# Kernel tuning notes

Measured on AMD Instinct MI355X. Metric: run time of the kernel, lower is better.

Reference implementation:

```python
import jax, jax.numpy as jnp
import numpy as np

B, T, K, H = 2, 4096, 512, 8


def setup_inputs() -> dict:
    key = jax.random.key(0)
    ks = jax.random.split(key, 6)
    scale = 1.0 / np.sqrt(K)
    return {
        "x": jax.random.normal(ks[0], (B, T, K), dtype=jnp.float32),
        "padding_mask": jnp.ones((B, T), dtype=jnp.int32),
        "Wq": jax.random.normal(ks[1], (K, K), dtype=jnp.float32) * scale,
        "Wk": jax.random.normal(ks[2], (K, K), dtype=jnp.float32) * scale,
        "Wv": jax.random.normal(ks[3], (K, K), dtype=jnp.float32) * scale,
        "Wu": jax.random.normal(ks[4], (K, K), dtype=jnp.float32) * scale,
        "bu": jnp.zeros((K,), dtype=jnp.float32),
    }


def reference(x, padding_mask, Wq, Wk, Wv, Wu, bu):
    b, t, e = x.shape
    h = H
    s = e // h
    # torch Linear: y = x @ W.T
    q = (x @ Wq.T).reshape(b, t, h, s).transpose(0, 2, 1, 3)  # (b,h,t,s)
    k = (x @ Wk.T).reshape(b, t, h, s).transpose(0, 2, 1, 3)
    v = (x @ Wv.T).reshape(b, t, h, s).transpose(0, 2, 1, 3)
    inv4 = e ** (-0.25)
    q = q * inv4
    k = k * inv4
    dot = jnp.einsum("bhqs,bhks->bhqk", q, k)  # (b,h,t,t)
    neg_inf = jnp.float32(-jnp.inf)
    # causal mask (self.mask == True)
    causal = jnp.triu(jnp.ones((t, t), dtype=bool), k=1)
    dot = jnp.where(causal[None, None], neg_inf, dot)
    # padding mask applied along the QUERY dimension, as in the original
    dot = jnp.where(padding_mask[:, None, :, None] == 0, neg_inf, dot)
    attn = jax.nn.softmax(dot, axis=-1)
    out = jnp.einsum("bhqk,bhks->bhqs", attn, v)  # (b,h,t,s)
    out = out.transpose(0, 2, 1, 3).reshape(b, t, e)
    return out @ Wu.T + bu
```

## Files before the change

### kernel.cpp

```cpp
#include <hip/hip_runtime.h>
#include <hip/hip_bf16.h>

#define BB 2
#define TT 4096
#define KK 512
#define HH 8
#define SS 64
#define MM 8192

typedef __attribute__((ext_vector_type(8))) short bf16x8;
typedef __attribute__((ext_vector_type(4))) float f32x4;
typedef unsigned int u32;
typedef __attribute__((ext_vector_type(2))) u32 u32x2;
typedef __attribute__((ext_vector_type(4))) u32 u32x4;

#define SCL_QK 0.25250488f

static __device__ __forceinline__ u32 cvt2(float lo, float hi) {
    u32 r;
    asm("v_cvt_pk_bf16_f32 %0, %1, %2" : "=v"(r) : "v"(lo), "v"(hi));
    return r;
}

#define GLOAD16(g, l) __builtin_amdgcn_global_load_lds( \
    (const __attribute__((address_space(1))) void*)(g), \
    (__attribute__((address_space(3))) void*)(l), 16, 0, 0)

static __device__ __forceinline__ int rho(int v) {
    return (v & 0x23) | ((v & 0x04) << 2) | ((v & 0x18) >> 1);
}

__global__ __launch_bounds__(256) void cvt_bf16(
    const float* __restrict__ x,
    const float* __restrict__ Wq, const float* __restrict__ Wk,
    const float* __restrict__ Wv, const float* __restrict__ Wu,
    short* __restrict__ xb, short* __restrict__ wb)
{
    const int NX = MM * KK;
    const int NW = KK * KK;
    int idx = blockIdx.x * blockDim.x + threadIdx.x;
    int total = (NX + 4 * NW) >> 3;
    for (int g = idx; g < total; g += gridDim.x * blockDim.x) {
        int e = g << 3;
        const float* src; short* dst; float scl = 1.0f;
        if (e < NX) { src = x + e; dst = xb + e; }
        else {
            int gg = e - NX;
            int wsel = gg >> 18;
            int off = gg & (NW - 1);
            src = (wsel == 0 ? Wq : wsel == 1 ? Wk : wsel == 2 ? Wv : Wu) + off;
            dst = wb + gg;
            if (wsel <= 1) scl = SCL_QK;
        }
        float4 a = *(const float4*)src;
        float4 b = *(const float4*)(src + 4);
        a.x *= scl; a.y *= scl; a.z *= scl; a.w *= scl;
        b.x *= scl; b.y *= scl; b.z *= scl; b.w *= scl;
        u32x4 wv = { cvt2(a.x, a.y), cvt2(a.z, a.w), cvt2(b.x, b.y), cvt2(b.z, b.w) };
        *(u32x4*)dst = wv;
    }
}

__global__ __launch_bounds__(256) void proj_qkv(
    const short* __restrict__ xb, const short* __restrict__ wb,
    short* __restrict__ q, short* __restrict__ k, short* __restrict__ v)
{
    __shared__ short aS[128 * 64];
    __shared__ short bS[128 * 64];
    int nt = blockIdx.x, mt = blockIdx.y, z = blockIdx.z;
    const short* W = wb + (size_t)z * KK * KK;
    short* dst = (z == 0) ? q : ((z == 1) ? k : v);
    bool tr = (z != 2);
    int tid = threadIdx.x, wave = tid >> 6, lane = tid & 63;
    int lr = lane & 15, lg = lane >> 4;
    int wr = wave >> 1, wc = wave & 1;
    int l8 = lane >> 3, c8 = lane & 7;

    const short* Ag = xb + (size_t)(mt * 128) * KK;
    const short* Bg = W + (size_t)(nt * 128) * KK;

    f32x4 acc[4][4];
#pragma unroll
    for (int m = 0; m < 4; ++m)
#pragma unroll
        for (int n = 0; n < 4; ++n) acc[m][n] = (f32x4){0.f, 0.f, 0.f, 0.f};

    for (int k0 = 0; k0 < KK; k0 += 64) {
        __syncthreads();
#pragma unroll
        for (int i = 0; i < 4; ++i) {
            int row = wave * 32 + i * 8 + l8;
            GLOAD16(Ag + (size_t)row * KK + k0 + c8 * 8, &aS[(wave * 32 + i * 8) * 64]);
            GLOAD16(Bg + (size_t)row * KK + k0 + c8 * 8, &bS[(wave * 32 + i * 8) * 64]);
        }
        __syncthreads();
#pragma unroll
        for (int kc = 0; kc < 2; ++kc) {
            bf16x8 af[4], bw[4];
#pragma unroll
            for (int m = 0; m < 4; ++m)
                af[m] = *(const bf16x8*)&aS[(wr * 64 + m * 16 + lr) * 64 + kc * 32 + lg * 8];
#pragma unroll
            for (int n = 0; n < 4; ++n)
                bw[n] = *(const bf16x8*)&bS[(wc * 64 + n * 16 + lr) * 64 + kc * 32 + lg * 8];
            if (tr) {
#pragma unroll
                for (int m = 0; m < 4; ++m)
#pragma unroll
                    for (int n = 0; n < 4; ++n)
                        acc[m][n] = __builtin_amdgcn_mfma_f32_16x16x32_bf16(bw[n], af[m], acc[m][n], 0, 0, 0);
            } else {
#pragma unroll
                for (int m = 0; m < 4; ++m)
#pragma unroll
                    for (int n = 0; n < 4; ++n)
                        acc[m][n] = __builtin_amdgcn_mfma_f32_16x16x32_bf16(af[m], bw[n], acc[m][n], 0, 0, 0);
            }
        }
    }

    if (tr) {
        int h = nt * 2 + wc;
#pragma unroll
        for (int n = 0; n < 4; ++n) {
            int s0 = n * 16 + lg * 4;
#pragma unroll
            for (int m = 0; m < 4; ++m) {
                int tg = mt * 128 + wr * 64 + m * 16 + lr;
                int b = tg >> 12, t = tg & (TT - 1);
                u32x2 pk = { cvt2(acc[m][n][0], acc[m][n][1]), cvt2(acc[m][n][2], acc[m][n][3]) };
                *(u32x2*)&dst[((size_t)(b * HH + h) * TT + t) * SS + s0] = pk;
            }
        }
    } else {
#pragma unroll
        for (int n = 0; n < 4; ++n) {
            int nn = nt * 128 + wc * 64 + n * 16 + lr;
            int h = nn >> 6, s = nn & 63;
#pragma unroll
            for (int m = 0; m < 4; ++m) {
                int m0 = mt * 128 + wr * 64 + m * 16 + lg * 4;
                int b = m0 >> 12, t0 = m0 & (TT - 1);
                u32x2 pk = { cvt2(acc[m][n][0], acc[m][n][1]), cvt2(acc[m][n][2], acc[m][n][3]) };
                *(u32x2*)&dst[(((size_t)(b * HH + h)) * SS + s) * TT + t0] = pk;
            }
        }
    }
}

__global__ __launch_bounds__(256) void proj_out(
    const short* __restrict__ a, const short* __restrict__ Wub,
    const float* __restrict__ bu, float* __restrict__ out)
{
    __shared__ short aS[64 * 64];
    __shared__ short bS[128 * 64];
    int nt = blockIdx.x, mt = blockIdx.y;
    int tid = threadIdx.x, wave = tid >> 6, lane = tid & 63;
    int lr = lane & 15, lg = lane >> 4;
    int wr = wave >> 1, wc = wave & 1;
    int l8 = lane >> 3, c8 = lane & 7;

    const short* Ag = a + (size_t)(mt * 64) * KK;
    const short* Bg = Wub + (size_t)(nt * 128) * KK;

    f32x4 acc[2][4];
#pragma unroll
    for (int m = 0; m < 2; ++m)
#pragma unroll
        for (int n = 0; n < 4; ++n) acc[m][n] = (f32x4){0.f, 0.f, 0.f, 0.f};

    for (int k0 = 0; k0 < KK; k0 += 64) {
        __syncthreads();
#pragma unroll
        for (int i = 0; i < 2; ++i) {
            int row = wave * 16 + i * 8 + l8;
            GLOAD16(Ag + (size_t)row * KK + k0 + c8 * 8, &aS[(wave * 16 + i * 8) * 64]);
        }
#pragma unroll
        for (int i = 0; i < 4; ++i) {
            int row = wave * 32 + i * 8 + l8;
            GLOAD16(Bg + (size_t)row * KK + k0 + c8 * 8, &bS[(wave * 32 + i * 8) * 64]);
        }
        __syncthreads();
#pragma unroll
        for (int kc = 0; kc < 2; ++kc) {
            bf16x8 af[2], bw[4];
#pragma unroll
            for (int m = 0; m < 2; ++m)
                af[m] = *(const bf16x8*)&aS[(wr * 32 + m * 16 + lr) * 64 + kc * 32 + lg * 8];
#pragma unroll
            for (int n = 0; n < 4; ++n)
                bw[n] = *(const bf16x8*)&bS[(wc * 64 + n * 16 + lr) * 64 + kc * 32 + lg * 8];
#pragma unroll
            for (int m = 0; m < 2; ++m)
#pragma unroll
                for (int n = 0; n < 4; ++n)
                    acc[m][n] = __builtin_amdgcn_mfma_f32_16x16x32_bf16(bw[n], af[m], acc[m][n], 0, 0, 0);
        }
    }

#pragma unroll
    for (int n = 0; n < 4; ++n) {
        int f0 = nt * 128 + wc * 64 + n * 16 + lg * 4;
        float4 bias4 = *(const float4*)&bu[f0];
#pragma unroll
        for (int m = 0; m < 2; ++m) {
            int t = mt * 64 + wr * 32 + m * 16 + lr;
            float4 ov = { acc[m][n][0] + bias4.x, acc[m][n][1] + bias4.y,
                          acc[m][n][2] + bias4.z, acc[m][n][3] + bias4.w };
            *(float4*)&out[(size_t)t * KK + f0] = ov;
        }
    }
}

__global__ __launch_bounds__(256) void flash_attn(
    const short* __restrict__ Q, const short* __restrict__ Kv,
    const short* __restrict__ Vt, short* __restrict__ Oout)
{
    __shared__ short k_lds[64][72];
    __shared__ short v_lds[64][72];

    int u = blockIdx.x;
    int xcd = u & 7, sblk = u >> 3;
    int bh = 2 * xcd + (sblk & 1);
    int i4 = sblk >> 1;
    int qt = (i4 < 16) ? (63 - i4) : (i4 < 32 ? (i4 - 16) : (i4 < 48 ? (79 - i4) : (i4 - 32)));

    int tid = threadIdx.x, wave = tid >> 6, lane = tid & 63;
    int lr = lane & 15, lg = lane >> 4;
    int b = bh >> 3, h = bh & 7;

    const short* Qb = Q + (size_t)bh * TT * SS;
    const short* Kb = Kv + (size_t)bh * TT * SS;
    const short* Vb = Vt + (size_t)bh * SS * TT;

    int urow = tid >> 3, useg = tid & 7;
    int kdr0 = rho(urow), kdr1 = rho(urow + 32);

    int qrow0 = qt * 64 + wave * 16;

    bf16x8 a_q[2];
#pragma unroll
    for (int kc = 0; kc < 2; ++kc)
        a_q[kc] = *(const bf16x8*)&Qb[(size_t)(qrow0 + lr) * SS + kc * 32 + lg * 8];

    f32x4 o[4];
#pragma unroll
    for (int n = 0; n < 4; ++n) o[n] = (f32x4){0.f, 0.f, 0.f, 0.f};
    float m_run = -INFINITY, l_run = 0.f;

    int nkv = qt + 1;
    bf16x8 kr0, kr1, vr0, vr1;
    kr0 = *(const bf16x8*)&Kb[(size_t)urow * SS + useg * 8];
    kr1 = *(const bf16x8*)&Kb[(size_t)(urow + 32) * SS + useg * 8];
    vr0 = *(const bf16x8*)&Vb[(size_t)urow * TT + useg * 8];
    vr1 = *(const bf16x8*)&Vb[(size_t)(urow + 32) * TT + useg * 8];

    for (int kt = 0; kt < nkv; ++kt) {
        __syncthreads();
        *(bf16x8*)&k_lds[kdr0][useg * 8]      = kr0;
        *(bf16x8*)&k_lds[kdr1][useg * 8]      = kr1;
        *(bf16x8*)&v_lds[urow][useg * 8]      = vr0;
        *(bf16x8*)&v_lds[urow + 32][useg * 8] = vr1;
        if (kt + 1 < nkv) {
            int kn = kt + 1;
            kr0 = *(const bf16x8*)&Kb[(size_t)(kn * 64 + urow) * SS + useg * 8];
            kr1 = *(const bf16x8*)&Kb[(size_t)(kn * 64 + urow + 32) * SS + useg * 8];
            vr0 = *(const bf16x8*)&Vb[(size_t)urow * TT + kn * 64 + useg * 8];
            vr1 = *(const bf16x8*)&Vb[(size_t)(urow + 32) * TT + kn * 64 + useg * 8];
        }
        __syncthreads();

        f32x4 sc[4];
#pragma unroll
        for (int ct = 0; ct < 4; ++ct) sc[ct] = (f32x4){0.f, 0.f, 0.f, 0.f};
        __builtin_amdgcn_s_setprio(1);
#pragma unroll
        for (int kc = 0; kc < 2; ++kc) {
#pragma unroll
            for (int ct = 0; ct < 4; ++ct) {
                bf16x8 kf = *(const bf16x8*)&k_lds[ct * 16 + lr][kc * 32 + lg * 8];
                sc[ct] = __builtin_amdgcn_mfma_f32_16x16x32_bf16(kf, a_q[kc], sc[ct], 0, 0, 0);
            }
        }
        __builtin_amdgcn_s_setprio(0);
        if (kt == qt) {
            int qq = qrow0 + lr;
#pragma unroll
            for (int ct = 0; ct < 4; ++ct) {
                int kv0 = kt * 64 + (ct >> 1) * 32 + lg * 8 + (ct & 1) * 4;
#pragma unroll
                for (int r = 0; r < 4; ++r)
                    if (kv0 + r > qq) sc[ct][r] = -INFINITY;
            }
        }
        float mx = -INFINITY;
#pragma unroll
        for (int ct = 0; ct < 4; ++ct)
#pragma unroll
            for (int r = 0; r < 4; ++r) mx = fmaxf(mx, sc[ct][r]);
        mx = fmaxf(mx, __shfl_xor(mx, 16));
        mx = fmaxf(mx, __shfl_xor(mx, 32));
        if (!__all(mx <= m_run + 8.0f)) {
            float mnew = fmaxf(m_run, mx);
            float corr = __builtin_amdgcn_exp2f(m_run - mnew);
            l_run *= corr;
#pragma unroll
            for (int st = 0; st < 4; ++st)
#pragma unroll
                for (int r = 0; r < 4; ++r) o[st][r] *= corr;
            m_run = mnew;
        }
        float s0 = 0.f;
#pragma unroll
        for (int ct = 0; ct < 4; ++ct)
#pragma unroll
            for (int r = 0; r < 4; ++r) {
                float pf = __builtin_amdgcn_exp2f(sc[ct][r] - m_run);
                sc[ct][r] = pf;
                s0 += pf;
            }
        s0 += __shfl_xor(s0, 16);
        s0 += __shfl_xor(s0, 32);
        l_run += s0;

        __builtin_amdgcn_s_setprio(1);
#pragma unroll
        for (int kc = 0; kc < 2; ++kc) {
            u32x4 pw = { cvt2(sc[2 * kc][0], sc[2 * kc][1]),
                         cvt2(sc[2 * kc][2], sc[2 * kc][3]),
                         cvt2(sc[2 * kc + 1][0], sc[2 * kc + 1][1]),
                         cvt2(sc[2 * kc + 1][2], sc[2 * kc + 1][3]) };
            bf16x8 pb = __builtin_bit_cast(bf16x8, pw);
#pragma unroll
            for (int st = 0; st < 4; ++st) {
                bf16x8 vf = *(const bf16x8*)&v_lds[st * 16 + lr][kc * 32 + lg * 8];
                o[st] = __builtin_amdgcn_mfma_f32_16x16x32_bf16(vf, pb, o[st], 0, 0, 0);
            }
        }
        __builtin_amdgcn_s_setprio(0);
    }

    float inv = 1.f / l_run;
    int t = qrow0 + lr;
#pragma unroll
    for (int st = 0; st < 4; ++st) {
        u32x2 ov = { cvt2(o[st][0] * inv, o[st][1] * inv), cvt2(o[st][2] * inv, o[st][3] * inv) };
        *(u32x2*)&Oout[(size_t)(b * TT + t) * KK + h * 64 + st * 16 + lg * 4] = ov;
    }
}

extern "C" void kernel_launch(void* const* d_in, const int* in_sizes, int n_in,
                              void* d_out, int out_size, void* d_ws, size_t ws_size,
                              hipStream_t stream) {
    const float* x  = (const float*)d_in[0];
    const float* Wq = (const float*)d_in[2];
    const float* Wk = (const float*)d_in[3];
    const float* Wv = (const float*)d_in[4];
    const float* Wu = (const float*)d_in[5];
    const float* bu = (const float*)d_in[6];
    float* out = (float*)d_out;

    short* q_ws  = (short*)d_ws;
    short* k_ws  = q_ws + (size_t)MM * KK;
    short* v_ws  = k_ws + (size_t)MM * KK;
    short* a_ws  = v_ws + (size_t)MM * KK;
    short* wb_ws = a_ws + (size_t)MM * KK;

    cvt_bf16<<<2560, 256, 0, stream>>>(x, Wq, Wk, Wv, Wu, a_ws, wb_ws);

    dim3 gQKV(KK / 128, MM / 128, 3);
    proj_qkv<<<gQKV, 256, 0, stream>>>(a_ws, wb_ws, q_ws, k_ws, v_ws);

    flash_attn<<<1024, 256, 0, stream>>>(q_ws, k_ws, v_ws, a_ws);

    dim3 gO(KK / 128, MM / 64);
    proj_out<<<gO, 256, 0, stream>>>(a_ws, wb_ws + 3 * (size_t)KK * KK, bu, out);
}
```

Baseline: 192.1 us.

## Double-buffer GEMM LDS loads with XOR swizzle; switch attention to 32x32 MFMA tiles

Both projection GEMMs get double-buffered LDS stages, so the next K-slice is fetched while the current one is multiplied. The LDS row segments are XOR-swizzled to avoid bank conflicts and one barrier per iteration is dropped. The flash attention kernel now uses 32x32x16 MFMA with 128-query tiles per block, which halves the grid and changes the causal tile scheduling and K swizzle. The costs are twice the LDS per block, more registers for the larger accumulators, and fewer blocks in the attention launch.

```diff
diff --git a/kernel.cpp b/kernel.cpp
--- a/kernel.cpp
+++ b/kernel.cpp
@@ -10,6 +10,7 @@
 
 typedef __attribute__((ext_vector_type(8))) short bf16x8;
 typedef __attribute__((ext_vector_type(4))) float f32x4;
+typedef __attribute__((ext_vector_type(16))) float f32x16;
 typedef unsigned int u32;
 typedef __attribute__((ext_vector_type(2))) u32 u32x2;
 typedef __attribute__((ext_vector_type(4))) u32 u32x4;
@@ -26,8 +27,8 @@
     (const __attribute__((address_space(1))) void*)(g), \
     (__attribute__((address_space(3))) void*)(l), 16, 0, 0)
 
-static __device__ __forceinline__ int rho(int v) {
-    return (v & 0x23) | ((v & 0x04) << 2) | ((v & 0x18) >> 1);
+static __device__ __forceinline__ int swap23(int v) {
+    return (v & ~12) | ((v & 4) << 1) | ((v & 8) >> 1);
 }
 
 __global__ __launch_bounds__(256) void cvt_bf16(
@@ -65,8 +66,8 @@
     const short* __restrict__ xb, const short* __restrict__ wb,
     short* __restrict__ q, short* __restrict__ k, short* __restrict__ v)
 {
-    __shared__ short aS[128 * 64];
-    __shared__ short bS[128 * 64];
+    __shared__ short aS[2][128 * 64];
+    __shared__ short bS[2][128 * 64];
     int nt = blockIdx.x, mt = blockIdx.y, z = blockIdx.z;
     const short* W = wb + (size_t)z * KK * KK;
     short* dst = (z == 0) ? q : ((z == 1) ? k : v);
@@ -74,7 +75,7 @@
     int tid = threadIdx.x, wave = tid >> 6, lane = tid & 63;
     int lr = lane & 15, lg = lane >> 4;
     int wr = wave >> 1, wc = wave & 1;
-    int l8 = lane >> 3, c8 = lane & 7;
+    int sri = lane >> 3, ss0 = lane & 7;
 
     const short* Ag = xb + (size_t)(mt * 128) * KK;
     const short* Bg = W + (size_t)(nt * 128) * KK;
@@ -85,24 +86,35 @@
 #pragma unroll
         for (int n = 0; n < 4; ++n) acc[m][n] = (f32x4){0.f, 0.f, 0.f, 0.f};
 
-    for (int k0 = 0; k0 < KK; k0 += 64) {
+    auto STAGE = [&](int buf, int k0) {
+#pragma unroll
+        for (int g = 0; g < 4; ++g) {
+            int R0 = wave * 32 + g * 8;
+            int srow = R0 + sri;
+            int sseg = ss0 ^ (srow & 7);
+            GLOAD16(Ag + (size_t)srow * KK + k0 + sseg * 8, &aS[buf][R0 * 64]);
+            GLOAD16(Bg + (size_t)srow * KK + k0 + sseg * 8, &bS[buf][R0 * 64]);
+        }
+    };
+
+    STAGE(0, 0);
+    int cur = 0;
+    for (int kt = 0; kt < 8; ++kt) {
         __syncthreads();
-#pragma unroll
-        for (int i = 0; i < 4; ++i) {
-            int row = wave * 32 + i * 8 + l8;
-            GLOAD16(Ag + (size_t)row * KK + k0 + c8 * 8, &aS[(wave * 32 + i * 8) * 64]);
-            GLOAD16(Bg + (size_t)row * KK + k0 + c8 * 8, &bS[(wave * 32 + i * 8) * 64]);
-        }
-        __syncthreads();
+        if (kt < 7) STAGE(cur ^ 1, (kt + 1) * 64);
+        bf16x8 af[4], bw[4];
 #pragma unroll
         for (int kc = 0; kc < 2; ++kc) {
-            bf16x8 af[4], bw[4];
-#pragma unroll
-            for (int m = 0; m < 4; ++m)
-                af[m] = *(const bf16x8*)&aS[(wr * 64 + m * 16 + lr) * 64 + kc * 32 + lg * 8];
-#pragma unroll
-            for (int n = 0; n < 4; ++n)
-                bw[n] = *(const bf16x8*)&bS[(wc * 64 + n * 16 + lr) * 64 + kc * 32 + lg * 8];
+#pragma unroll
+            for (int m = 0; m < 4; ++m) {
+                int row = wr * 64 + m * 16 + lr;
+                af[m] = *(const bf16x8*)&aS[cur][row * 64 + ((4 * kc + lg) ^ (row & 7)) * 8];
+            }
+#pragma unroll
+            for (int n = 0; n < 4; ++n) {
+                int row = wc * 64 + n * 16 + lr;
+                bw[n] = *(const bf16x8*)&bS[cur][row * 64 + ((4 * kc + lg) ^ (row & 7)) * 8];
+            }
             if (tr) {
 #pragma unroll
                 for (int m = 0; m < 4; ++m)
@@ -117,6 +129,7 @@
                         acc[m][n] = __builtin_amdgcn_mfma_f32_16x16x32_bf16(af[m], bw[n], acc[m][n], 0, 0, 0);
             }
         }
+        cur ^= 1;
     }
 
     if (tr) {
@@ -152,13 +165,13 @@
     const short* __restrict__ a, const short* __restrict__ Wub,
     const float* __restrict__ bu, float* __restrict__ out)
 {
-    __shared__ short aS[64 * 64];
-    __shared__ short bS[128 * 64];
+    __shared__ short aS[2][64 * 64];
+    __shared__ short bS[2][128 * 64];
     int nt = blockIdx.x, mt = blockIdx.y;
     int tid = threadIdx.x, wave = tid >> 6, lane = tid & 63;
     int lr = lane & 15, lg = lane >> 4;
     int wr = wave >> 1, wc = wave & 1;
-    int l8 = lane >> 3, c8 = lane & 7;
+    int sri = lane >> 3, ss0 = lane & 7;
 
     const short* Ag = a + (size_t)(mt * 64) * KK;
     const short* Bg = Wub + (size_t)(nt * 128) * KK;
@@ -169,34 +182,48 @@
 #pragma unroll
         for (int n = 0; n < 4; ++n) acc[m][n] = (f32x4){0.f, 0.f, 0.f, 0.f};
 
-    for (int k0 = 0; k0 < KK; k0 += 64) {
+    auto STAGE = [&](int buf, int k0) {
+#pragma unroll
+        for (int g = 0; g < 2; ++g) {
+            int R0 = wave * 16 + g * 8;
+            int srow = R0 + sri;
+            int sseg = ss0 ^ (srow & 7);
+            GLOAD16(Ag + (size_t)srow * KK + k0 + sseg * 8, &aS[buf][R0 * 64]);
+        }
+#pragma unroll
+        for (int g = 0; g < 4; ++g) {
+            int R0 = wave * 32 + g * 8;
+            int srow = R0 + sri;
+            int sseg = ss0 ^ (srow & 7);
+            GLOAD16(Bg + (size_t)srow * KK + k0 + sseg * 8, &bS[buf][R0 * 64]);
+        }
+    };
+
+    STAGE(0, 0);
+    int cur = 0;
+    for (int kt = 0; kt < 8; ++kt) {
         __syncthreads();
-#pragma unroll
-        for (int i = 0; i < 2; ++i) {
-            int row = wave * 16 + i * 8 + l8;
-            GLOAD16(Ag + (size_t)row * KK + k0 + c8 * 8, &aS[(wave * 16 + i * 8) * 64]);
-        }
-#pragma unroll
-        for (int i = 0; i < 4; ++i) {
-            int row = wave * 32 + i * 8 + l8;
-            GLOAD16(Bg + (size_t)row * KK + k0 + c8 * 8, &bS[(wave * 32 + i * 8) * 64]);
-        }
-        __syncthreads();
+        if (kt < 7) STAGE(cur ^ 1, (kt + 1) * 64);
+        bf16x8 af[2], bw[4];
 #pragma unroll
         for (int kc = 0; kc < 2; ++kc) {
-            bf16x8 af[2], bw[4];
-#pragma unroll
-            for (int m = 0; m < 2; ++m)
-                af[m] = *(const bf16x8*)&aS[(wr * 32 + m * 16 + lr) * 64 + kc * 32 + lg * 8];
-#pragma unroll
-            for (int n = 0; n < 4; ++n)
-                bw[n] = *(const bf16x8*)&bS[(wc * 64 + n * 16 + lr) * 64 + kc * 32 + lg * 8];
+#pragma unroll
+            for (int m = 0; m < 2; ++m) {
+                int row = wr * 32 + m * 16 + lr;
+                af[m] = *(const bf16x8*)&aS[cur][row * 64 + ((4 * kc + lg) ^ (row & 7)) * 8];
+            }
+#pragma unroll
+            for (int n = 0; n < 4; ++n) {
+                int row = wc * 64 + n * 16 + lr;
+                bw[n] = *(const bf16x8*)&bS[cur][row * 64 + ((4 * kc + lg) ^ (row & 7)) * 8];
+            }
 #pragma unroll
             for (int m = 0; m < 2; ++m)
 #pragma unroll
                 for (int n = 0; n < 4; ++n)
                     acc[m][n] = __builtin_amdgcn_mfma_f32_16x16x32_bf16(bw[n], af[m], acc[m][n], 0, 0, 0);
         }
+        cur ^= 1;
     }
 
 #pragma unroll
@@ -221,13 +248,13 @@
     __shared__ short v_lds[64][72];
 
     int u = blockIdx.x;
-    int xcd = u & 7, sblk = u >> 3;
-    int bh = 2 * xcd + (sblk & 1);
-    int i4 = sblk >> 1;
-    int qt = (i4 < 16) ? (63 - i4) : (i4 < 32 ? (i4 - 16) : (i4 < 48 ? (79 - i4) : (i4 - 32)));
+    int xcd = u & 7, r = u >> 3;
+    int bh = 2 * xcd + (r & 1);
+    int qi = (r >> 1) & 15;
+    int qt = (r >> 5) ? (16 + qi) : (15 - qi);
 
     int tid = threadIdx.x, wave = tid >> 6, lane = tid & 63;
-    int lr = lane & 15, lg = lane >> 4;
+    int l32 = lane & 31, hi = lane >> 5;
     int b = bh >> 3, h = bh & 7;
 
     const short* Qb = Q + (size_t)bh * TT * SS;
@@ -235,21 +262,24 @@
     const short* Vb = Vt + (size_t)bh * SS * TT;
 
     int urow = tid >> 3, useg = tid & 7;
-    int kdr0 = rho(urow), kdr1 = rho(urow + 32);
-
-    int qrow0 = qt * 64 + wave * 16;
-
-    bf16x8 a_q[2];
-#pragma unroll
-    for (int kc = 0; kc < 2; ++kc)
-        a_q[kc] = *(const bf16x8*)&Qb[(size_t)(qrow0 + lr) * SS + kc * 32 + lg * 8];
-
-    f32x4 o[4];
-#pragma unroll
-    for (int n = 0; n < 4; ++n) o[n] = (f32x4){0.f, 0.f, 0.f, 0.f};
+    int sr0 = swap23(urow), sr1 = sr0 + 32;
+
+    int qbase = qt * 128 + wave * 32;
+    int qrow = qbase + l32;
+
+    bf16x8 bq[4];
+#pragma unroll
+    for (int c = 0; c < 4; ++c)
+        bq[c] = *(const bf16x8*)&Qb[(size_t)qrow * SS + c * 16 + hi * 8];
+
+    f32x16 oa[2];
+#pragma unroll
+    for (int T = 0; T < 2; ++T)
+#pragma unroll
+        for (int rr = 0; rr < 16; ++rr) oa[T][rr] = 0.f;
     float m_run = -INFINITY, l_run = 0.f;
 
-    int nkv = qt + 1;
+    int nkv = 2 * qt + 2;
     bf16x8 kr0, kr1, vr0, vr1;
     kr0 = *(const bf16x8*)&Kb[(size_t)urow * SS + useg * 8];
     kr1 = *(const bf16x8*)&Kb[(size_t)(urow + 32) * SS + useg * 8];
@@ -258,8 +288,8 @@
 
     for (int kt = 0; kt < nkv; ++kt) {
         __syncthreads();
-        *(bf16x8*)&k_lds[kdr0][useg * 8]      = kr0;
-        *(bf16x8*)&k_lds[kdr1][useg * 8]      = kr1;
+        *(bf16x8*)&k_lds[sr0][useg * 8]       = kr0;
+        *(bf16x8*)&k_lds[sr1][useg * 8]       = kr1;
         *(bf16x8*)&v_lds[urow][useg * 8]      = vr0;
         *(bf16x8*)&v_lds[urow + 32][useg * 8] = vr1;
         if (kt + 1 < nkv) {
@@ -271,83 +301,88 @@
         }
         __syncthreads();
 
-        f32x4 sc[4];
-#pragma unroll
-        for (int ct = 0; ct < 4; ++ct) sc[ct] = (f32x4){0.f, 0.f, 0.f, 0.f};
+        f32x16 sa[2];
+#pragma unroll
+        for (int T = 0; T < 2; ++T)
+#pragma unroll
+            for (int rr = 0; rr < 16; ++rr) sa[T][rr] = 0.f;
         __builtin_amdgcn_s_setprio(1);
 #pragma unroll
-        for (int kc = 0; kc < 2; ++kc) {
-#pragma unroll
-            for (int ct = 0; ct < 4; ++ct) {
-                bf16x8 kf = *(const bf16x8*)&k_lds[ct * 16 + lr][kc * 32 + lg * 8];
-                sc[ct] = __builtin_amdgcn_mfma_f32_16x16x32_bf16(kf, a_q[kc], sc[ct], 0, 0, 0);
-            }
+        for (int c = 0; c < 4; ++c) {
+            bf16x8 a0 = *(const bf16x8*)&k_lds[l32][c * 16 + hi * 8];
+            bf16x8 a1 = *(const bf16x8*)&k_lds[l32 + 32][c * 16 + hi * 8];
+            sa[0] = __builtin_amdgcn_mfma_f32_32x32x16_bf16(a0, bq[c], sa[0], 0, 0, 0);
+            sa[1] = __builtin_amdgcn_mfma_f32_32x32x16_bf16(a1, bq[c], sa[1], 0, 0, 0);
         }
         __builtin_amdgcn_s_setprio(0);
-        if (kt == qt) {
-            int qq = qrow0 + lr;
-#pragma unroll
-            for (int ct = 0; ct < 4; ++ct) {
-                int kv0 = kt * 64 + (ct >> 1) * 32 + lg * 8 + (ct & 1) * 4;
-#pragma unroll
-                for (int r = 0; r < 4; ++r)
-                    if (kv0 + r > qq) sc[ct][r] = -INFINITY;
-            }
-        }
+
+        if (kt >= 2 * qt) {
+#pragma unroll
+            for (int T = 0; T < 2; ++T)
+#pragma unroll
+                for (int rr = 0; rr < 16; ++rr) {
+                    int kv = kt * 64 + (rr & 3) + 4 * ((rr >> 2) & 1) + 8 * hi
+                           + 16 * (rr >> 3) + 32 * T;
+                    if (kv > qrow) sa[T][rr] = -INFINITY;
+                }
+        }
+
         float mx = -INFINITY;
 #pragma unroll
-        for (int ct = 0; ct < 4; ++ct)
-#pragma unroll
-            for (int r = 0; r < 4; ++r) mx = fmaxf(mx, sc[ct][r]);
-        mx = fmaxf(mx, __shfl_xor(mx, 16));
+        for (int T = 0; T < 2; ++T)
+#pragma unroll
+            for (int rr = 0; rr < 16; ++rr) mx = fmaxf(mx, sa[T][rr]);
         mx = fmaxf(mx, __shfl_xor(mx, 32));
         if (!__all(mx <= m_run + 8.0f)) {
             float mnew = fmaxf(m_run, mx);
             float corr = __builtin_amdgcn_exp2f(m_run - mnew);
             l_run *= corr;
 #pragma unroll
-            for (int st = 0; st < 4; ++st)
-#pragma unroll
-                for (int r = 0; r < 4; ++r) o[st][r] *= corr;
+            for (int T = 0; T < 2; ++T)
+#pragma unroll
+                for (int rr = 0; rr < 16; ++rr) oa[T][rr] *= corr;
             m_run = mnew;
         }
         float s0 = 0.f;
 #pragma unroll
-        for (int ct = 0; ct < 4; ++ct)
-#pragma unroll
-            for (int r = 0; r < 4; ++r) {
-                float pf = __builtin_amdgcn_exp2f(sc[ct][r] - m_run);
-                sc[ct][r] = pf;
+        for (int T = 0; T < 2; ++T)
+#pragma unroll
+            for (int rr = 0; rr < 16; ++rr) {
+                float pf = __builtin_amdgcn_exp2f(sa[T][rr] - m_run);
+                sa[T][rr] = pf;
                 s0 += pf;
             }
-        s0 += __shfl_xor(s0, 16);
         s0 += __shfl_xor(s0, 32);
         l_run += s0;
 
         __builtin_amdgcn_s_setprio(1);
 #pragma unroll
-        for (int kc = 0; kc < 2; ++kc) {
-            u32x4 pw = { cvt2(sc[2 * kc][0], sc[2 * kc][1]),
-                         cvt2(sc[2 * kc][2], sc[2 * kc][3]),
-                         cvt2(sc[2 * kc + 1][0], sc[2 * kc + 1][1]),
-                         cvt2(sc[2 * kc + 1][2], sc[2 * kc + 1][3]) };
+        for (int c = 0; c < 4; ++c) {
+            const int T = c >> 1, base = 8 * (c & 1);
+            u32x4 pw = { cvt2(sa[T][base + 0], sa[T][base + 1]),
+                         cvt2(sa[T][base + 2], sa[T][base + 3]),
+                         cvt2(sa[T][base + 4], sa[T][base + 5]),
+                         cvt2(sa[T][base + 6], sa[T][base + 7]) };
             bf16x8 pb = __builtin_bit_cast(bf16x8, pw);
-#pragma unroll
-            for (int st = 0; st < 4; ++st) {
-                bf16x8 vf = *(const bf16x8*)&v_lds[st * 16 + lr][kc * 32 + lg * 8];
-                o[st] = __builtin_amdgcn_mfma_f32_16x16x32_bf16(vf, pb, o[st], 0, 0, 0);
-            }
+            bf16x8 av0 = *(const bf16x8*)&v_lds[l32][c * 16 + hi * 8];
+            bf16x8 av1 = *(const bf16x8*)&v_lds[l32 + 32][c * 16 + hi * 8];
+            oa[0] = __builtin_amdgcn_mfma_f32_32x32x16_bf16(av0, pb, oa[0], 0, 0, 0);
+            oa[1] = __builtin_amdgcn_mfma_f32_32x32x16_bf16(av1, pb, oa[1], 0, 0, 0);
         }
         __builtin_amdgcn_s_setprio(0);
     }
 
     float inv = 1.f / l_run;
-    int t = qrow0 + lr;
-#pragma unroll
-    for (int st = 0; st < 4; ++st) {
-        u32x2 ov = { cvt2(o[st][0] * inv, o[st][1] * inv), cvt2(o[st][2] * inv, o[st][3] * inv) };
-        *(u32x2*)&Oout[(size_t)(b * TT + t) * KK + h * 64 + st * 16 + lg * 4] = ov;
-    }
+    short* dp = Oout + (size_t)(b * TT + qrow) * KK + h * 64;
+#pragma unroll
+    for (int St = 0; St < 2; ++St)
+#pragma unroll
+        for (int qd = 0; qd < 4; ++qd) {
+            int s0i = 32 * St + 8 * qd + 4 * hi;
+            u32x2 ov = { cvt2(oa[St][4 * qd + 0] * inv, oa[St][4 * qd + 1] * inv),
+                         cvt2(oa[St][4 * qd + 2] * inv, oa[St][4 * qd + 3] * inv) };
+            *(u32x2*)&dp[s0i] = ov;
+        }
 }
 
 extern "C" void kernel_launch(void* const* d_in, const int* in_sizes, int n_in,
@@ -372,7 +407,7 @@
     dim3 gQKV(KK / 128, MM / 128, 3);
     proj_qkv<<<gQKV, 256, 0, stream>>>(a_ws, wb_ws, q_ws, k_ws, v_ws);
 
-    flash_attn<<<1024, 256, 0, stream>>>(q_ws, k_ws, v_ws, a_ws);
+    flash_attn<<<512, 256, 0, stream>>>(q_ws, k_ws, v_ws, a_ws);
 
     dim3 gO(KK / 128, MM / 64);
     proj_out<<<gO, 256, 0, stream>>>(a_ws, wb_ws + 3 * (size_t)KK * KK, bu, out);
```

New measurement: 191.2 us. Within noise of the previous version (-0.5%).
